# Optimization experiments

Hardware: AMD Instinct MI355X
Metric: run time of the kernel (lower is better)

The kernel has to match this reference:

```python
import jax, jax.numpy as jnp
import numpy as np

N = 100000   # nodes
E = 800000   # edges
H = 128      # hidden_dim
HOP = 3
B = 64       # graphs


def setup_inputs() -> dict:
    key = jax.random.key(0)
    ks = jax.random.split(key, 24)
    s = 0.05
    x = jnp.round(jax.random.uniform(ks[0], (N, 1))).astype(jnp.float32)  # binary node indicator
    edge_index = jax.random.randint(ks[1], (2, E), 0, N)
    edge_attr = jax.random.normal(ks[2], (E, 1), dtype=jnp.float32)
    batch = jnp.sort(jax.random.randint(ks[3], (N,), 0, B))
    p = lambda k, sh: (s * jax.random.normal(k, sh)).astype(jnp.float32)
    return dict(
        x=x, edge_index=edge_index, edge_attr=edge_attr, batch=batch, num_graphs=B,
        l0_w=p(ks[4], (HOP, 1, H)), l0_b=p(ks[5], (HOP, H)),
        l1_w=p(ks[6], (HOP, H, H)), l1_b=p(ks[7], (HOP, H)),
        l2_w=p(ks[8], (HOP, 1, H)), l2_b=p(ks[9], (HOP, H)),
        l3_w=p(ks[10], (HOP, 1, 1)), l3_b=p(ks[11], (HOP, 1)),
        att_w=p(ks[12], (2 * H, H)), att_b=p(ks[13], (H,)),
        sp_w=p(ks[14], (H, H)), sp_b=p(ks[15], (H,)),
        ac_w=p(ks[16], (2 * H, H)), ac_b=p(ks[17], (H,)),
        last_w=p(ks[18], (2 * H, 1)), last_b=p(ks[19], (1,)),
    )


def _seg_mean(v, idx, m):
    # scatter-mean into m buckets; empty buckets -> 0 (matches PyG MeanAggregation)
    s = jax.ops.segment_sum(v, idx, num_segments=m)
    c = jax.ops.segment_sum(jnp.ones((v.shape[0], 1), v.dtype), idx, num_segments=m)
    return jnp.where(c > 0, s / jnp.maximum(c, 1.0), 0.0)


def reference(x, edge_index, edge_attr, batch, num_graphs,
              l0_w, l0_b, l1_w, l1_b, l2_w, l2_b, l3_w, l3_b,
              att_w, att_b, sp_w, sp_b, ac_w, ac_b, last_w, last_b):
    n = x.shape[0]
    row, col = edge_index[0], edge_index[1]
    hop, hid = l0_w.shape[0], l0_w.shape[2]
    u = jnp.zeros((n, hid), x.dtype)
    for i in range(hop):
        first = x @ l0_w[i] + l0_b[i]                      # [N,H]
        u_agg = _seg_mean(edge_attr * u[col], row, n)      # gather + scatter-mean
        second = u_agg @ l1_w[i] + l1_b[i]
        ee = jax.nn.relu(edge_attr @ l3_w[i] + l3_b[i])    # [E,1]
        third = _seg_mean(ee, row, n) @ l2_w[i] + l2_b[i]
        u = jax.nn.relu(first + second + third)
    # per-graph cluster embeddings (global_mean_pool ratios)
    h_c_0 = _seg_mean(u * (1 - x), batch, num_graphs) / _seg_mean(1 - x, batch, num_graphs)
    h_c_1 = _seg_mean(u * x, batch, num_graphs) / _seg_mean(x, batch, num_graphs)
    hc0, hc1 = h_c_0[batch], h_c_1[batch]                  # [N,H]
    tce = x * hc0 + (1 - x) * hc1
    h_a = jnp.concatenate([u, tce], axis=-1)               # [N,2H]
    att = h_a @ att_w + att_b
    w0 = jnp.sum(att * hc0, axis=1, keepdims=True)
    w1 = jnp.sum(att * hc1, axis=1, keepdims=True)
    w = jax.nn.softmax(jnp.concatenate([w0, w1], axis=-1), axis=-1)
    h_s = w[:, :1] * hc0 + w[:, 1:] * hc1
    q = jnp.concatenate([h_s @ sp_w + sp_b, h_a @ ac_w + ac_b], axis=-1) @ last_w + last_b
    return q
```

## Files before the change

### kernel.cpp

```cpp
#include <hip/hip_runtime.h>
#include <stdint.h>

typedef unsigned int  u32;
typedef unsigned short u16;
typedef unsigned char u8;

typedef short bf16x8 __attribute__((ext_vector_type(8)));
typedef float f32x4  __attribute__((ext_vector_type(4)));
typedef float f32x2  __attribute__((ext_vector_type(2)));

static __device__ __forceinline__ float b2f(u16 h){
    union { u32 u; float f; } v; v.u = ((u32)h) << 16; return v.f;
}
static __device__ __forceinline__ float b2f_hi(u32 w){
    union { u32 u; float f; } v; v.u = w & 0xFFFF0000u; return v.f;
}
static __device__ __forceinline__ float b2f_lo(u32 w){
    union { u32 u; float f; } v; v.u = w << 16; return v.f;
}
static __device__ __forceinline__ u16 f2b(float f){
    union { float f; u32 u; } v; v.f = f;
    u32 r = v.u + 0x7FFFu + ((v.u >> 16) & 1u);
    return (u16)(r >> 16);
}
static __device__ __forceinline__ u32 cvt_pk(float lo, float hi){
    u32 r; asm("v_cvt_pk_bf16_f32 %0, %1, %2" : "=v"(r) : "v"(lo), "v"(hi));
    return r;
}
static __device__ __forceinline__ u16 f2b1(float f){
    u32 r; asm("v_cvt_pk_bf16_f32 %0, %1, %2" : "=v"(r) : "v"(f), "v"(f));
    return (u16)r;
}

#define USCALE 64.0f
static __device__ __forceinline__ u32 pk8_lo(float a, float b, u32 old){
    return __builtin_amdgcn_cvt_pk_fp8_f32(a, b, old, false);
}
static __device__ __forceinline__ u32 pk8_hi(float a, float b, u32 old){
    return __builtin_amdgcn_cvt_pk_fp8_f32(a, b, old, true);
}
#define ACCF8(acc, g, v) { \
    f32x2 _a = __builtin_amdgcn_cvt_pk_f32_fp8((int)(v).x, false); \
    f32x2 _b = __builtin_amdgcn_cvt_pk_f32_fp8((int)(v).x, true);  \
    f32x2 _c = __builtin_amdgcn_cvt_pk_f32_fp8((int)(v).y, false); \
    f32x2 _d = __builtin_amdgcn_cvt_pk_f32_fp8((int)(v).y, true);  \
    acc[0] += g * _a[0]; acc[1] += g * _a[1]; \
    acc[2] += g * _b[0]; acc[3] += g * _b[1]; \
    acc[4] += g * _c[0]; acc[5] += g * _c[1]; \
    acc[6] += g * _d[0]; acc[7] += g * _d[1]; }

#define ACCP(acc, g, sv) { \
    u32 _bb = __float_as_uint(sv); \
    float _t = __uint_as_float(_bb & 0x7FFFFFFFu); \
    bool _x = (_bb >> 31) != 0u; \
    _Pragma("unroll") \
    for (int _k = 0; _k < 8; ++_k){ \
        float _v = fmaxf(fmaf(_t, cl2[_k], _x ? cb1[_k] : cb0[_k]), 0.f); \
        acc[_k] = fmaf(g, _v, acc[_k]); } }

#define OL0W 0
#define OL0B 384
#define OL1W 768
#define OL1B 49920
#define OL2W 50304
#define OL2B 50688
#define OL3W 51072
#define OL3B 51075
#define OATTW 51078
#define OATTB 83846
#define OSPW 83974
#define OSPB 100358
#define OACW 100486
#define OACB 133254
#define OLASTW 133382
#define OLASTB 133638
#define WTOT 133639

#define PREPW_BLOCKS 192
#define ECAP 40

struct Ptrs16 { const void* p[16]; };

static __device__ __forceinline__ int detect_bf(const u32* __restrict__ xw){
    int lane = threadIdx.x & 63;
    int f = 0;
    #pragma unroll
    for (int i = 0; i < 8; ++i){
        u32 w = xw[lane * 8 + i];
        f |= ((w & 0xFFFFu) == 0x3F80u) ? 1 : 0;
    }
    return __ballot(f) != 0ull;
}

__global__ __launch_bounds__(256) void k_prep(Ptrs16 wp, const void* __restrict__ xin,
                                              float* __restrict__ wc, float* __restrict__ xc,
                                              u16* __restrict__ w1t, float* __restrict__ basev,
                                              int* __restrict__ flag,
                                              const int* __restrict__ row, const int* __restrict__ col,
                                              const void* __restrict__ ea,
                                              int* __restrict__ cnt, int2* __restrict__ ecs,
                                              int scatBase, int E, int N){
    int b = blockIdx.x, t = threadIdx.x;
    int bf = detect_bf((const u32*)xin);
    if (b >= scatBase){
        int e0 = ((b - scatBase) * 256 + t) * 4;
        if (e0 >= E) return;
        int rr[4], cc[4]; float av[4];
        if (e0 + 3 < E){
            int4 rv = *(const int4*)(row + e0);
            int4 cv = *(const int4*)(col + e0);
            rr[0]=rv.x; rr[1]=rv.y; rr[2]=rv.z; rr[3]=rv.w;
            cc[0]=cv.x; cc[1]=cv.y; cc[2]=cv.z; cc[3]=cv.w;
            if (bf){
                ushort4 ev = *(const ushort4*)((const u16*)ea + e0);
                av[0]=b2f(ev.x); av[1]=b2f(ev.y); av[2]=b2f(ev.z); av[3]=b2f(ev.w);
            } else {
                float4 ev = *(const float4*)((const float*)ea + e0);
                av[0]=ev.x; av[1]=ev.y; av[2]=ev.z; av[3]=ev.w;
            }
        } else {
            #pragma unroll
            for (int j = 0; j < 4; ++j){
                int e = e0 + j;
                rr[j] = (e < E) ? row[e] : 0;
                cc[j] = (e < E) ? col[e] : 0;
                av[j] = (e < E) ? (bf ? b2f(((const u16*)ea)[e]) : ((const float*)ea)[e]) : 0.f;
            }
        }
        int slot[4];
        #pragma unroll
        for (int j = 0; j < 4; ++j)
            slot[j] = (e0 + j < E) ? atomicAdd(&cnt[rr[j]], 1) : ECAP;
        #pragma unroll
        for (int j = 0; j < 4; ++j)
            if (e0 + j < E && slot[j] < ECAP)
                ecs[(size_t)rr[j] * ECAP + slot[j]] = make_int2(cc[j], __float_as_int(av[j]));
        return;
    }
    auto rd = [&](int seg, int off) -> float {
        return bf ? b2f(((const u16*)wp.p[seg])[off]) : ((const float*)wp.p[seg])[off];
    };
    if (b < PREPW_BLOCKS){
        int id = b * 256 + t;
        int i = id >> 14, rem = id & 16383;
        int n = rem >> 7, k = rem & 127;
        w1t[(i * 128 + n) * 128 + k] = f2b(rd(2, (i * 128 + k) * 128 + n));
        if (id < 384) basev[id] = rd(1, id) + rd(3, id) + rd(5, id);
        if (id == 0) *flag = bf;
    } else {
        int i = (b - PREPW_BLOCKS) * 256 + t;
        const int sz[16] = {384,384,49152,384,384,384,3,3,32768,128,16384,128,32768,128,256,1};
        if (i < WTOT){
            int seg = 0, off = i;
            while (off >= sz[seg]){ off -= sz[seg]; ++seg; }
            wc[i] = rd(seg, off);
        } else {
            int n = i - WTOT;
            if (n < N) xc[n] = bf ? b2f(((const u16*)xin)[n]) : ((const float*)xin)[n];
        }
    }
}

__global__ __launch_bounds__(256) void k_hop0(const int2* __restrict__ ecs, const int* __restrict__ cnt,
                                              const float* __restrict__ xc, const float* __restrict__ wc,
                                              float* __restrict__ t12, float* __restrict__ spf,
                                              float* __restrict__ acf, float* __restrict__ biasv,
                                              float* __restrict__ xt0, int foldBlk, int N){
    if ((int)blockIdx.x == foldBlk){
        int t = threadIdx.x;
        const float* aw  = wc + OACW + t * 128;
        const float* lw2 = wc + OLASTW + 128;
        float s = 0.f;
        #pragma unroll 8
        for (int o = 0; o < 128; ++o) s += aw[o] * lw2[o];
        acf[t] = s;
        if (t < 128){
            const float* sw = wc + OSPW + t * 128;
            const float* lw = wc + OLASTW;
            float s2 = 0.f;
            #pragma unroll 8
            for (int o = 0; o < 128; ++o) s2 += sw[o] * lw[o];
            spf[t] = s2;
        }
        float pb = 0.f;
        if (t < 128) pb = wc[OSPB + t] * wc[OLASTW + t] + wc[OACB + t] * wc[OLASTW + 128 + t];
        __shared__ float red[4];
        #pragma unroll
        for (int m = 1; m < 64; m <<= 1) pb += __shfl_xor(pb, m);
        if ((t & 63) == 0) red[t >> 6] = pb;
        __syncthreads();
        if (t == 0) biasv[0] = red[0] + red[1] + red[2] + red[3] + wc[OLASTB];
        return;
    }
    int id = blockIdx.x * 256 + threadIdx.x;
    int n = id >> 4;
    if (n >= N) return;
    int sl = threadIdx.x & 15;
    float w30 = wc[OL3W + 0], w31 = wc[OL3W + 1], w32 = wc[OL3W + 2];
    float c30 = wc[OL3B + 0], c31 = wc[OL3B + 1], c32 = wc[OL3B + 2];
    int d = min(cnt[n], ECAP);
    size_t s = (size_t)n * ECAP;
    float s0 = 0.f, s1 = 0.f, s2 = 0.f;
    for (int e = sl; e < d; e += 16){
        float a = __int_as_float(ecs[s + e].y);
        s0 += fmaxf(a * w30 + c30, 0.f);
        s1 += fmaxf(a * w31 + c31, 0.f);
        s2 += fmaxf(a * w32 + c32, 0.f);
    }
    #pragma unroll
    for (int m = 1; m < 16; m <<= 1){
        s0 += __shfl_xor(s0, m);
        s1 += __shfl_xor(s1, m);
        s2 += __shfl_xor(s2, m);
    }
    float iv = d > 0 ? 1.0f / (float)d : 0.f;
    if (sl == 0){
        t12[n] = s1 * iv; t12[N + n] = s2 * iv;
        u32 tb = __float_as_uint(s0 * iv) | (xc[n] > 0.5f ? 0x80000000u : 0u);
        ((u32*)xt0)[n] = tb;
    }
}

template<int POOL, int OUTF8, int INPARAM>
__global__ __launch_bounds__(256) void k_hop(const void* __restrict__ uPrevV, void* __restrict__ uNext,
    const int2* __restrict__ ecs, const int* __restrict__ cnt,
    const u16* __restrict__ w1t, const float* __restrict__ basev,
    const float* __restrict__ l0wc, const float* __restrict__ l2wc,
    const float* __restrict__ p0c, const float* __restrict__ p2c, const float* __restrict__ pbc,
    const float* __restrict__ xc, const float* __restrict__ t_i,
    const int* __restrict__ batch, float* __restrict__ S0, float* __restrict__ S1,
    int* __restrict__ cnt1, int N)
{
    __shared__ __align__(16) u16 A[32][136];
    __shared__ __align__(8) int2 esh[32][17];
    __shared__ int dsh[32];
    int tid = threadIdx.x;
    int lane = tid & 63, wid = tid >> 6;
    int n0 = blockIdx.x * 32;
    int cid = lane & 15, grp = lane >> 4;
    const u8* uPrev = (const u8*)uPrevV;
    const float* xt0 = (const float*)uPrevV;

    float cl2[8], cb0[8], cb1[8];
    if (INPARAM){
        #pragma unroll
        for (int k = 0; k < 8; ++k){
            int ch = cid * 8 + k;
            cl2[k] = p2c[ch];
            float b = pbc[ch];
            cb0[k] = b; cb1[k] = b + p0c[ch];
        }
    }

    {
        int sr = tid >> 3, sl = tid & 7;
        int sn = n0 + sr;
        if (sn < N){
            int d = min(cnt[sn], ECAP);
            size_t sb = (size_t)sn * ECAP;
            int2 a = ecs[sb + sl];
            int2 b = ecs[sb + sl + 8];
            if (sl >= d)     a = make_int2(0, 0);
            if (sl + 8 >= d) b = make_int2(0, 0);
            esh[sr][sl]     = a;
            esh[sr][sl + 8] = b;
            if (sl == 0) dsh[sr] = d;
        } else {
            esh[sr][sl]     = make_int2(0, 0);
            esh[sr][sl + 8] = make_int2(0, 0);
            if (sl == 0) dsh[sr] = 0;
        }
    }

#define BATCH4(eb) { \
    int2 m0 = esh[r][(eb)], m1 = esh[r][(eb)+1], m2 = esh[r][(eb)+2], m3 = esh[r][(eb)+3]; \
    float g0 = __int_as_float(m0.y), g1 = __int_as_float(m1.y); \
    float g2 = __int_as_float(m2.y), g3 = __int_as_float(m3.y); \
    if (INPARAM){ \
        float q0 = xt0[m0.x], q1 = xt0[m1.x], q2 = xt0[m2.x], q3 = xt0[m3.x]; \
        ACCP(acc, g0, q0); ACCP(acc, g1, q1); ACCP(acc, g2, q2); ACCP(acc, g3, q3); \
    } else { \
        uint2 p0 = *(const uint2*)(uPrev + (size_t)m0.x * 128 + cid * 8); \
        uint2 p1 = *(const uint2*)(uPrev + (size_t)m1.x * 128 + cid * 8); \
        uint2 p2 = *(const uint2*)(uPrev + (size_t)m2.x * 128 + cid * 8); \
        uint2 p3 = *(const uint2*)(uPrev + (size_t)m3.x * 128 + cid * 8); \
        ACCF8(acc, g0, p0); ACCF8(acc, g1, p1); ACCF8(acc, g2, p2); ACCF8(acc, g3, p3); \
    } }

    #pragma unroll
    for (int p = 0; p < 2; ++p){
        int r = wid * 8 + p * 4 + grp;
        int n = n0 + r;
        float acc[8];
        #pragma unroll
        for (int j = 0; j < 8; ++j) acc[j] = 0.f;
        if (n < N){
            int d = dsh[r];
            BATCH4(0); BATCH4(4);
            if (__any(d > 8)){
                BATCH4(8); BATCH4(12);
            }
            if (d > 16){
                size_t s = (size_t)n * ECAP;
                for (int e = 16; e < d; ++e){
                    int2 mm = ecs[s + e];
                    float g = __int_as_float(mm.y);
                    if (INPARAM){
                        float q = xt0[mm.x];
                        ACCP(acc, g, q);
                    } else {
                        uint2 pp = *(const uint2*)(uPrev + (size_t)mm.x * 128 + cid * 8);
                        ACCF8(acc, g, pp);
                    }
                }
            }
            float sc = d > 0 ? (INPARAM ? 1.0f / (float)d : 1.0f / (USCALE * (float)d)) : 0.f;
            uint4 o;
            o.x = cvt_pk(acc[0] * sc, acc[1] * sc);
            o.y = cvt_pk(acc[2] * sc, acc[3] * sc);
            o.z = cvt_pk(acc[4] * sc, acc[5] * sc);
            o.w = cvt_pk(acc[6] * sc, acc[7] * sc);
            *(uint4*)&A[r][cid * 8] = o;
        } else {
            *(uint4*)&A[r][cid * 8] = make_uint4(0u, 0u, 0u, 0u);
        }
    }
#undef BATCH4
    __syncthreads();

    bf16x8 bfr[4][2];
    #pragma unroll
    for (int kk = 0; kk < 4; ++kk)
        #pragma unroll
        for (int nt = 0; nt < 2; ++nt)
            bfr[kk][nt] = *(const bf16x8*)(w1t + (size_t)(wid * 32 + nt * 16 + cid) * 128 + kk * 32 + grp * 8);

    f32x4 acc4[2][2];
    #pragma unroll
    for (int mt = 0; mt < 2; ++mt)
        #pragma unroll
        for (int nt = 0; nt < 2; ++nt) acc4[mt][nt] = (f32x4){0.f, 0.f, 0.f, 0.f};
    #pragma unroll
    for (int kk = 0; kk < 4; ++kk){
        int kb = kk * 32 + grp * 8;
        bf16x8 af[2];
        #pragma unroll
        for (int mt = 0; mt < 2; ++mt) af[mt] = *(const bf16x8*)&A[mt * 16 + cid][kb];
        #pragma unroll
        for (int mt = 0; mt < 2; ++mt)
            #pragma unroll
            for (int nt = 0; nt < 2; ++nt)
                acc4[mt][nt] = __builtin_amdgcn_mfma_f32_16x16x32_bf16(af[mt], bfr[kk][nt], acc4[mt][nt], 0, 0, 0);
    }

    float w0c[2], w2c[2], bc[2]; int colv[2];
    #pragma unroll
    for (int nt = 0; nt < 2; ++nt){
        int col = wid * 32 + nt * 16 + cid;
        colv[nt] = col;
        w0c[nt] = l0wc[col]; w2c[nt] = l2wc[col]; bc[nt] = basev[col];
    }
    int gLo = 0, gHi = 0;
    float accP[8];
    if (POOL){
        gLo = batch[n0];
        gHi = batch[min(n0 + 31, N - 1)];
        #pragma unroll
        for (int j = 0; j < 8; ++j) accP[j] = 0.f;
    }
    #pragma unroll
    for (int mt = 0; mt < 2; ++mt){
        #pragma unroll
        for (int rg = 0; rg < 4; ++rg){
            int n = n0 + mt * 16 + grp * 4 + rg;
            if (n < N){
                float xv = xc[n];
                float tv = t_i[n];
                int sel = 0;
                if (POOL){
                    sel = ((batch[n] != gLo) ? 2 : 0) + ((xv > 0.5f) ? 1 : 0);
                }
                #pragma unroll
                for (int nt = 0; nt < 2; ++nt){
                    float v = fmaxf(acc4[mt][nt][rg] + xv * w0c[nt] + tv * w2c[nt] + bc[nt], 0.f);
                    if (OUTF8){
                        u32 pk = pk8_lo(v * USCALE, v * USCALE, 0u);
                        ((u8*)uNext)[(size_t)n * 128 + colv[nt]] = (u8)pk;
                    } else {
                        ((u16*)uNext)[(size_t)n * 128 + colv[nt]] = f2b1(v);
                    }
                    if (POOL) accP[nt * 4 + sel] += v;
                }
            }
        }
    }
    if (POOL){
        #pragma unroll
        for (int j = 0; j < 8; ++j){
            accP[j] += __shfl_xor(accP[j], 16);
            accP[j] += __shfl_xor(accP[j], 32);
        }
        if (grp == 0){
            #pragma unroll
            for (int nt = 0; nt < 2; ++nt){
                atomicAdd(&S0[gLo * 128 + colv[nt]], accP[nt * 4 + 0]);
                atomicAdd(&S1[gLo * 128 + colv[nt]], accP[nt * 4 + 1]);
                if (gHi != gLo){
                    atomicAdd(&S0[gHi * 128 + colv[nt]], accP[nt * 4 + 2]);
                    atomicAdd(&S1[gHi * 128 + colv[nt]], accP[nt * 4 + 3]);
                }
            }
        }
        if (wid == 0){
            int n = n0 + lane;
            int ok = (lane < 32 && n < N) ? 1 : 0;
            int is1 = ok && (xc[n] > 0.5f);
            int hi  = ok && (batch[n] != gLo);
            unsigned long long mLo = __ballot(is1 && !hi);
            unsigned long long mHi = __ballot(is1 && hi);
            if (lane == 0){
                int c = __popcll(mLo);
                if (c) atomicAdd(&cnt1[gLo], c);
                c = __popcll(mHi);
                if (c && gHi != gLo) atomicAdd(&cnt1[gHi], c);
            }
        }
    }
}


static __device__ __forceinline__ int lowbound(const int* b, int n, int g){
    int lo = 0, hi = n;
    while (lo < hi){ int m = (lo + hi) >> 1; if (b[m] < g) lo = m + 1; else hi = m; }
    return lo;
}

__global__ __launch_bounds__(256) void k_graph(const float* __restrict__ S0, const float* __restrict__ S1,
                                               const int* __restrict__ cnt1, const int* __restrict__ batch,
                                               const float* __restrict__ wc, const float* __restrict__ spf,
                                               const float* __restrict__ acf,
                                               float* __restrict__ v0, float* __restrict__ v1,
                                               float* __restrict__ gsc, int N){
    __shared__ float h0[128], h1[128], sv0[128], sv1[128];
    int g = blockIdx.x, t = threadIdx.x;
    int st = lowbound(batch, N, g), en = lowbound(batch, N, g + 1);
    int c1 = cnt1[g], c0 = (en - st) - c1;
    if (t < 128){
        h0[t] = c0 > 0 ? S0[g * 128 + t] / (float)c0 : 0.f;
        h1[t] = c1 > 0 ? S1[g * 128 + t] / (float)c1 : 0.f;
    }
    __syncthreads();
    float a0 = 0.f, a1 = 0.f;
    for (int o = 0; o < 128; ++o){
        float w = wc[OATTW + t * 128 + o];
        a0 += w * h0[o];
        a1 += w * h1[o];
    }
    v0[g * 256 + t] = a0; v1[g * 256 + t] = a1;
    if (t >= 128){ sv0[t - 128] = a0; sv1[t - 128] = a1; }
    __syncthreads();
    if (t < 64){
        int l = t;
        float p[10];
        #pragma unroll
        for (int k = 0; k < 10; ++k) p[k] = 0.f;
        #pragma unroll
        for (int rep = 0; rep < 2; ++rep){
            int o = l + rep * 64;
            float hh0 = h0[o], hh1 = h1[o];
            float q0 = sv0[o], q1 = sv1[o];
            float ab = wc[OATTB + o];
            float sf = spf[o], af = acf[128 + o];
            p[0] += q0 * hh0; p[1] += q0 * hh1;
            p[2] += q1 * hh0; p[3] += q1 * hh1;
            p[4] += ab * hh0; p[5] += ab * hh1;
            p[6] += sf * hh0; p[7] += sf * hh1;
            p[8] += af * hh0; p[9] += af * hh1;
        }
        #pragma unroll
        for (int m = 1; m < 64; m <<= 1){
            #pragma unroll
            for (int k = 0; k < 10; ++k) p[k] += __shfl_xor(p[k], m);
        }
        if (l == 0){
            #pragma unroll
            for (int k = 0; k < 10; ++k) gsc[g * 10 + k] = p[k];
        }
    }
}

__global__ __launch_bounds__(256) void k_final(const u16* __restrict__ u, const float* __restrict__ xc,
                                               const int* __restrict__ batch,
                                               const float* __restrict__ v0, const float* __restrict__ v1,
                                               const float* __restrict__ acf, const float* __restrict__ gsc,
                                               const float* __restrict__ biasv, const int* __restrict__ flag,
                                               void* __restrict__ out, int N){
    int bf = *flag;
    int lane = threadIdx.x & 63, wid = threadIdx.x >> 6;
    int sub = lane >> 4, cid = lane & 15;
    int n = blockIdx.x * 16 + wid * 4 + sub;
    if (n >= N) return;
    int g = batch[n];
    int ch = cid * 8;
    uint4 uv = *(const uint4*)(u + (size_t)n * 128 + ch);
    const float* pv0 = v0 + g * 256 + ch;
    const float* pv1 = v1 + g * 256 + ch;
    const float* pac = acf + ch;
    float uu[8] = {b2f_lo(uv.x), b2f_hi(uv.x), b2f_lo(uv.y), b2f_hi(uv.y),
                   b2f_lo(uv.z), b2f_hi(uv.z), b2f_lo(uv.w), b2f_hi(uv.w)};
    float r0 = 0.f, r1 = 0.f, rA = 0.f;
    #pragma unroll
    for (int j = 0; j < 8; ++j){ r0 += uu[j] * pv0[j]; r1 += uu[j] * pv1[j]; rA += uu[j] * pac[j]; }
    #pragma unroll
    for (int m = 1; m < 16; m <<= 1){
        r0 += __shfl_xor(r0, m);
        r1 += __shfl_xor(r1, m);
        rA += __shfl_xor(rA, m);
    }
    if (cid == 0){
        const float* G = gsc + g * 10;
        bool xv = xc[n] > 0.5f;
        float z0 = r0 + (xv ? G[0] : G[1]) + G[4];
        float z1 = r1 + (xv ? G[2] : G[3]) + G[5];
        float mz = fmaxf(z0, z1);
        float e0 = expf(z0 - mz), e1 = expf(z1 - mz);
        float inv = 1.f / (e0 + e1);
        float q = (e0 * G[6] + e1 * G[7]) * inv + rA + (xv ? G[8] : G[9]) + biasv[0];
        if (bf) ((u16*)out)[n] = f2b(q);
        else    ((float*)out)[n] = q;
    }
}


extern "C" void kernel_launch(void* const* d_in, const int* in_sizes, int n_in,
                              void* d_out, int out_size, void* d_ws, size_t ws_size,
                              hipStream_t stream)
{
    const void* x    = d_in[0];
    const int* ei    = (const int*)d_in[1];
    const void* ea   = d_in[2];
    const int* batch = (const int*)d_in[3];
    Ptrs16 wp;
    for (int i = 0; i < 16; ++i) wp.p[i] = d_in[5 + i];

    int N = in_sizes[0];
    int E = in_sizes[2];
    const int* rowI = ei;
    const int* colI = ei + E;

    char* w = (char*)d_ws;
    size_t o = 0;
    auto alloc = [&](size_t b) -> char* {
        char* p = w + o; o = (o + b + 255) & ~(size_t)255; return p;
    };
    int*   flag   = (int*)alloc(4);
    float* basev  = (float*)alloc(3 * 128 * 4);
    float* spf    = (float*)alloc(128 * 4);
    float* acf    = (float*)alloc(256 * 4);
    float* biasv  = (float*)alloc(4);
    float* gsc    = (float*)alloc(64 * 10 * 4);
    float* v0     = (float*)alloc(64 * 256 * 4);
    float* v1     = (float*)alloc(64 * 256 * 4);
    float* wc     = (float*)alloc((size_t)WTOT * 4);
    float* xc     = (float*)alloc((size_t)N * 4);
    float* t12    = (float*)alloc((size_t)2 * N * 4);
    float* xt0    = (float*)alloc((size_t)N * 4);
    u16*   w1t    = (u16*)alloc((size_t)3 * 128 * 128 * 2);
    u16*   uA     = (u16*)alloc((size_t)N * 128 * 2);
    u8*    uB     = (u8*)alloc((size_t)N * 128);
    int2*  ecs    = (int2*)alloc((size_t)N * ECAP * 8);
    int*   cnt    = (int*)alloc((size_t)N * 4);
    float* S0     = (float*)alloc(64 * 128 * 4);
    float* S1     = (float*)alloc(64 * 128 * 4);
    int*   cnt1   = (int*)alloc(64 * 4);
    (void)ws_size; (void)n_in; (void)out_size;

    hipMemsetAsync(cnt, 0, (size_t)((char*)cnt1 - (char*)cnt) + 64 * 4, stream);

    int gE4 = (E / 4 + 255) / 256 + 1;
    int canonB = (WTOT + N + 255) / 256;
    int scatBase = PREPW_BLOCKS + canonB;

    k_prep<<<scatBase + gE4, 256, 0, stream>>>(wp, x, wc, xc, w1t, basev, flag,
                                               rowI, colI, ea, cnt, ecs, scatBase, E, N);
    int gHop0 = (N * 16 + 255) / 256;
    k_hop0<<<gHop0 + 1, 256, 0, stream>>>(ecs, cnt, xc, wc, t12, spf, acf, biasv,
                                          xt0, gHop0, N);

    int gHop = (N + 31) / 32;
    k_hop<0, 1, 1><<<gHop, 256, 0, stream>>>(xt0, uB, ecs, cnt,
                                             w1t + 1 * 16384, basev + 128, wc + OL0W + 128, wc + OL2W + 128,
                                             wc + OL0W, wc + OL2W, basev,
                                             xc, t12, batch, S0, S1, cnt1, N);
    k_hop<1, 0, 0><<<gHop, 256, 0, stream>>>(uB, uA, ecs, cnt,
                                             w1t + 2 * 16384, basev + 256, wc + OL0W + 256, wc + OL2W + 256,
                                             wc + OL0W, wc + OL2W, basev,
                                             xc, t12 + N, batch, S0, S1, cnt1, N);

    k_graph<<<64, 256, 0, stream>>>(S0, S1, cnt1, batch, wc, spf, acf, v0, v1, gsc, N);
    k_final<<<(N + 15) / 16, 256, 0, stream>>>(uA, xc, batch, v0, v1, acf, gsc, biasv, flag, d_out, N);
}
```

Before: 278.1 us.

## Build per-row edge lists via two-pass binned scatter with LDS atomics

Edge-list construction is reworked. Edges are first counting-sorted into coarse bins of 256 destination rows, using LDS histograms and one global atomic per bin per block. A second kernel then scatters each bin into the per-row ECAP slots with shared-memory atomics and computes the hop-0 edge-MLP means in the same pass, replacing the separate k_hop0 kernel. This removes per-edge global atomics and scattered writes, at the cost of an extra intermediate buffer round trip. Bins that exceed the fixed bcap capacity, or rows that reach column indices at or above 2^24, would be silently truncated.

```diff
diff --git a/kernel.cpp b/kernel.cpp
--- a/kernel.cpp
+++ b/kernel.cpp
@@ -98,43 +98,43 @@
                                               int* __restrict__ flag,
                                               const int* __restrict__ row, const int* __restrict__ col,
                                               const void* __restrict__ ea,
-                                              int* __restrict__ cnt, int2* __restrict__ ecs,
-                                              int scatBase, int E, int N){
+                                              int2* __restrict__ binbuf, int* __restrict__ bcnt,
+                                              int scatBase, int E, int N, int nbin, int bcap){
     int b = blockIdx.x, t = threadIdx.x;
     int bf = detect_bf((const u32*)xin);
     if (b >= scatBase){
-        int e0 = ((b - scatBase) * 256 + t) * 4;
-        if (e0 >= E) return;
-        int rr[4], cc[4]; float av[4];
-        if (e0 + 3 < E){
-            int4 rv = *(const int4*)(row + e0);
-            int4 cv = *(const int4*)(col + e0);
-            rr[0]=rv.x; rr[1]=rv.y; rr[2]=rv.z; rr[3]=rv.w;
-            cc[0]=cv.x; cc[1]=cv.y; cc[2]=cv.z; cc[3]=cv.w;
-            if (bf){
-                ushort4 ev = *(const ushort4*)((const u16*)ea + e0);
-                av[0]=b2f(ev.x); av[1]=b2f(ev.y); av[2]=b2f(ev.z); av[3]=b2f(ev.w);
-            } else {
-                float4 ev = *(const float4*)((const float*)ea + e0);
-                av[0]=ev.x; av[1]=ev.y; av[2]=ev.z; av[3]=ev.w;
+        __shared__ int lcnt[512];
+        __shared__ int gbase[512];
+        int blockBase = (b - scatBase) * 4096;
+        for (int i = t; i < nbin; i += 256) lcnt[i] = 0;
+        __syncthreads();
+        #pragma unroll
+        for (int r = 0; r < 16; ++r){
+            int e = blockBase + r * 256 + t;
+            if (e < E) atomicAdd(&lcnt[row[e] >> 8], 1);
+        }
+        __syncthreads();
+        for (int i = t; i < nbin; i += 256){
+            int c = lcnt[i];
+            gbase[i] = c ? atomicAdd(&bcnt[i], c) : 0;
+            lcnt[i] = 0;
+        }
+        __syncthreads();
+        #pragma unroll
+        for (int r = 0; r < 16; ++r){
+            int e = blockBase + r * 256 + t;
+            if (e < E){
+                int rw = row[e];
+                int cl = col[e];
+                float a = bf ? b2f(((const u16*)ea)[e]) : ((const float*)ea)[e];
+                int bin = rw >> 8;
+                int sl = atomicAdd(&lcnt[bin], 1);
+                int idx = gbase[bin] + sl;
+                if (idx < bcap)
+                    binbuf[(size_t)bin * bcap + idx] =
+                        make_int2(((rw & 255) << 24) | cl, __float_as_int(a));
             }
-        } else {
-            #pragma unroll
-            for (int j = 0; j < 4; ++j){
-                int e = e0 + j;
-                rr[j] = (e < E) ? row[e] : 0;
-                cc[j] = (e < E) ? col[e] : 0;
-                av[j] = (e < E) ? (bf ? b2f(((const u16*)ea)[e]) : ((const float*)ea)[e]) : 0.f;
-            }
-        }
-        int slot[4];
-        #pragma unroll
-        for (int j = 0; j < 4; ++j)
-            slot[j] = (e0 + j < E) ? atomicAdd(&cnt[rr[j]], 1) : ECAP;
-        #pragma unroll
-        for (int j = 0; j < 4; ++j)
-            if (e0 + j < E && slot[j] < ECAP)
-                ecs[(size_t)rr[j] * ECAP + slot[j]] = make_int2(cc[j], __float_as_int(av[j]));
+        }
         return;
     }
     auto rd = [&](int seg, int off) -> float {
@@ -161,13 +161,16 @@
     }
 }
 
-__global__ __launch_bounds__(256) void k_hop0(const int2* __restrict__ ecs, const int* __restrict__ cnt,
-                                              const float* __restrict__ xc, const float* __restrict__ wc,
-                                              float* __restrict__ t12, float* __restrict__ spf,
-                                              float* __restrict__ acf, float* __restrict__ biasv,
-                                              float* __restrict__ xt0, int foldBlk, int N){
-    if ((int)blockIdx.x == foldBlk){
-        int t = threadIdx.x;
+__global__ __launch_bounds__(256) void k_binscat(const int2* __restrict__ binbuf,
+                                                 const int* __restrict__ bcnt,
+                                                 const float* __restrict__ wc, const float* __restrict__ xc,
+                                                 int2* __restrict__ ecs, int* __restrict__ cnt,
+                                                 float* __restrict__ t12, float* __restrict__ xt0,
+                                                 float* __restrict__ spf, float* __restrict__ acf,
+                                                 float* __restrict__ biasv,
+                                                 int nbin, int bcap, int N){
+    int b = blockIdx.x, t = threadIdx.x;
+    if (b == nbin){
         const float* aw  = wc + OACW + t * 128;
         const float* lw2 = wc + OLASTW + 128;
         float s = 0.f;
@@ -192,31 +195,36 @@
         if (t == 0) biasv[0] = red[0] + red[1] + red[2] + red[3] + wc[OLASTB];
         return;
     }
-    int id = blockIdx.x * 256 + threadIdx.x;
-    int n = id >> 4;
-    if (n >= N) return;
-    int sl = threadIdx.x & 15;
+    __shared__ int lcnt[256];
+    __shared__ float s0s[256], s1s[256], s2s[256];
+    lcnt[t] = 0; s0s[t] = 0.f; s1s[t] = 0.f; s2s[t] = 0.f;
+    __syncthreads();
+    int nbase = b << 8;
+    int ecnt = min(bcnt[b], bcap);
     float w30 = wc[OL3W + 0], w31 = wc[OL3W + 1], w32 = wc[OL3W + 2];
     float c30 = wc[OL3B + 0], c31 = wc[OL3B + 1], c32 = wc[OL3B + 2];
-    int d = min(cnt[n], ECAP);
-    size_t s = (size_t)n * ECAP;
-    float s0 = 0.f, s1 = 0.f, s2 = 0.f;
-    for (int e = sl; e < d; e += 16){
-        float a = __int_as_float(ecs[s + e].y);
-        s0 += fmaxf(a * w30 + c30, 0.f);
-        s1 += fmaxf(a * w31 + c31, 0.f);
-        s2 += fmaxf(a * w32 + c32, 0.f);
-    }
-    #pragma unroll
-    for (int m = 1; m < 16; m <<= 1){
-        s0 += __shfl_xor(s0, m);
-        s1 += __shfl_xor(s1, m);
-        s2 += __shfl_xor(s2, m);
-    }
-    float iv = d > 0 ? 1.0f / (float)d : 0.f;
-    if (sl == 0){
-        t12[n] = s1 * iv; t12[N + n] = s2 * iv;
-        u32 tb = __float_as_uint(s0 * iv) | (xc[n] > 0.5f ? 0x80000000u : 0u);
+    const int2* bb = binbuf + (size_t)b * bcap;
+    for (int e = t; e < ecnt; e += 256){
+        int2 v = bb[e];
+        int rowIn = (int)(((u32)v.x) >> 24);
+        int cl = v.x & 0xFFFFFF;
+        float a = __int_as_float(v.y);
+        int sl = atomicAdd(&lcnt[rowIn], 1);
+        if (sl < ECAP)
+            ecs[(size_t)(nbase + rowIn) * ECAP + sl] = make_int2(cl, v.y);
+        atomicAdd(&s0s[rowIn], fmaxf(a * w30 + c30, 0.f));
+        atomicAdd(&s1s[rowIn], fmaxf(a * w31 + c31, 0.f));
+        atomicAdd(&s2s[rowIn], fmaxf(a * w32 + c32, 0.f));
+    }
+    __syncthreads();
+    int n = nbase + t;
+    if (n < N){
+        int c = lcnt[t];
+        cnt[n] = c;
+        float iv = c > 0 ? 1.0f / (float)c : 0.f;
+        t12[n] = s1s[t] * iv;
+        t12[N + n] = s2s[t] * iv;
+        u32 tb = __float_as_uint(s0s[t] * iv) | (xc[n] > 0.5f ? 0x80000000u : 0u);
         ((u32*)xt0)[n] = tb;
     }
 }
@@ -548,6 +556,9 @@
     const int* rowI = ei;
     const int* colI = ei + E;
 
+    int nbin = (N + 255) >> 8;
+    int bcap = E / nbin + E / (nbin * 4) + 128;
+
     char* w = (char*)d_ws;
     size_t o = 0;
     auto alloc = [&](size_t b) -> char* {
@@ -569,23 +580,25 @@
     u16*   uA     = (u16*)alloc((size_t)N * 128 * 2);
     u8*    uB     = (u8*)alloc((size_t)N * 128);
     int2*  ecs    = (int2*)alloc((size_t)N * ECAP * 8);
+    int2*  binbuf = (int2*)alloc((size_t)nbin * bcap * 8);
     int*   cnt    = (int*)alloc((size_t)N * 4);
     float* S0     = (float*)alloc(64 * 128 * 4);
     float* S1     = (float*)alloc(64 * 128 * 4);
     int*   cnt1   = (int*)alloc(64 * 4);
+    int*   bcnt   = (int*)alloc((size_t)nbin * 4);
     (void)ws_size; (void)n_in; (void)out_size;
 
-    hipMemsetAsync(cnt, 0, (size_t)((char*)cnt1 - (char*)cnt) + 64 * 4, stream);
-
-    int gE4 = (E / 4 + 255) / 256 + 1;
+    hipMemsetAsync(cnt, 0, (size_t)((char*)bcnt - (char*)cnt) + (size_t)nbin * 4, stream);
+
     int canonB = (WTOT + N + 255) / 256;
     int scatBase = PREPW_BLOCKS + canonB;
-
-    k_prep<<<scatBase + gE4, 256, 0, stream>>>(wp, x, wc, xc, w1t, basev, flag,
-                                               rowI, colI, ea, cnt, ecs, scatBase, E, N);
-    int gHop0 = (N * 16 + 255) / 256;
-    k_hop0<<<gHop0 + 1, 256, 0, stream>>>(ecs, cnt, xc, wc, t12, spf, acf, biasv,
-                                          xt0, gHop0, N);
+    int gA = (E + 4095) / 4096;
+
+    k_prep<<<scatBase + gA, 256, 0, stream>>>(wp, x, wc, xc, w1t, basev, flag,
+                                              rowI, colI, ea, binbuf, bcnt,
+                                              scatBase, E, N, nbin, bcap);
+    k_binscat<<<nbin + 1, 256, 0, stream>>>(binbuf, bcnt, wc, xc, ecs, cnt, t12, xt0,
+                                            spf, acf, biasv, nbin, bcap, N);
 
     int gHop = (N + 31) / 32;
     k_hop<0, 1, 1><<<gHop, 256, 0, stream>>>(xt0, uB, ecs, cnt,
```

Measured after the change: 260.5 us. 1.07x faster.
